# Performance work log

Hardware: AMD Instinct MI355X
Metric: run time of the kernel (lower is better)

Reference implementation:

```python
import jax, jax.numpy as jnp
import numpy as np

EPS = 1e-5

def _silu(x):
    return x * jax.nn.sigmoid(x)

def _layernorm(x, g, b):
    mu = jnp.mean(x, axis=-1, keepdims=True)
    var = jnp.mean((x - mu) ** 2, axis=-1, keepdims=True)
    return (x - mu) * jax.lax.rsqrt(var + EPS) * g + b

def _mamba(x, in_w, conv_w, conv_b, xproj_w, dt_w, dt_b, A_log, Dp, out_w):
    # x: (B, L, dm); faithful mamba-ssm block: in_proj -> causal dwconv -> silu ->
    # x_proj -> softplus(dt_proj) -> selective scan -> gate -> out_proj
    B, L, dm = x.shape
    di, K = conv_w.shape          # d_inner, d_conv
    ds = A_log.shape[1]           # d_state
    dtr = dt_w.shape[1]           # dt_rank
    xz = x @ in_w.T               # (B, L, 2*di)
    xi, z = jnp.split(xz, 2, axis=-1)
    # causal depthwise conv1d (pad K-1 on the left), kernel unrolled (K=4)
    xpad = jnp.pad(xi, ((0, 0), (K - 1, 0), (0, 0)))
    xc = conv_b + sum(conv_w[:, k] * xpad[:, k:k + L, :] for k in range(K))
    xc = _silu(xc)                # (B, L, di)
    xdbl = xc @ xproj_w.T         # (B, L, dtr + 2*ds)
    dt, Bm, Cm = jnp.split(xdbl, [dtr, dtr + ds], axis=-1)
    delta = jax.nn.softplus(dt @ dt_w.T + dt_b)        # (B, L, di)
    A = -jnp.exp(A_log)                                # (di, ds)
    dA = jnp.exp(delta[..., None] * A)                 # (B, L, di, ds)
    dBu = delta[..., None] * Bm[:, :, None, :] * xc[..., None]
    def step(h, inp):
        dA_t, dBu_t, C_t = inp                         # (B,di,ds),(B,di,ds),(B,ds)
        h = dA_t * h + dBu_t
        y = jnp.einsum('bdn,bn->bd', h, C_t)
        return h, y
    h0 = jnp.zeros((B, di, ds), dtype=x.dtype)
    _, ys = jax.lax.scan(step, h0, (dA.transpose(1, 0, 2, 3),
                                    dBu.transpose(1, 0, 2, 3),
                                    Cm.transpose(1, 0, 2)))
    y = ys.transpose(1, 0, 2) + xc * Dp                # (B, L, di)
    y = y * _silu(z)
    return y @ out_w.T                                 # (B, L, dm)

def _forward(t1, t2, t3, t4, t5,
             m0_in_w, m0_conv_w, m0_conv_b, m0_xproj_w, m0_dt_w, m0_dt_b, m0_Alog, m0_D, m0_out_w,
             m1_in_w, m1_conv_w, m1_conv_b, m1_xproj_w, m1_dt_w, m1_dt_b, m1_Alog, m1_D, m1_out_w,
             norm_g, norm_b, proj_w, proj_b, norm1_g, norm1_b, proj1_w, proj1_b, skip_scale):
    B = t1.shape[0]
    flat = lambda t, c: t.reshape(B, c, -1).transpose(0, 2, 1)   # (B, N, C)
    f1, f2, f3, f4, f5 = flat(t1, 8), flat(t2, 16), flat(t3, 24), flat(t4, 32), flat(t5, 48)
    c1 = jnp.concatenate([f1[:, :, 0:8], f2[:, :, 0:8], f3[:, :, 0:8], f4[:, :, 0:8], f5[:, :, 0:8]], axis=1)   # (B,21824,8)
    c2 = jnp.concatenate([f2[:, :, 8:16], f3[:, :, 8:16], f4[:, :, 8:16], f5[:, :, 8:16]], axis=1)              # (B,5440,8)
    c3 = jnp.concatenate([f3[:, :, 16:24], f4[:, :, 16:24], f5[:, :, 16:24]], axis=1)                           # (B,1344,8)
    c4 = jnp.concatenate([f4[:, :, 24:32], f5[:, :, 24:32]], axis=1)                                            # (B,320,8)
    c5 = f5[:, :, 32:48]                                                                                        # (B,64,16)
    def block8(c):
        y = _mamba(c, m0_in_w, m0_conv_w, m0_conv_b, m0_xproj_w, m0_dt_w, m0_dt_b, m0_Alog, m0_D, m0_out_w)
        return _layernorm(y + skip_scale * c, norm_g, norm_b) @ proj_w.T + proj_b
    x1m, x2m, x3m, x4m = block8(c1), block8(c2), block8(c3), block8(c4)
    y5 = _mamba(c5, m1_in_w, m1_conv_w, m1_conv_b, m1_xproj_w, m1_dt_w, m1_dt_b, m1_Alog, m1_D, m1_out_w)
    x5m = _layernorm(y5 + skip_scale * c5, norm1_g, norm1_b) @ proj1_w.T + proj1_b
    a1 = x1m[:, 0:16384, :]
    a2 = jnp.concatenate([x1m[:, 16384:20480, :], x2m[:, 0:4096, :]], axis=2)
    a3 = jnp.concatenate([x1m[:, 20480:21504, :], x2m[:, 4096:5120, :], x3m[:, 0:1024, :]], axis=2)
    a4 = jnp.concatenate([x1m[:, 21504:21760, :], x2m[:, 5120:5376, :], x3m[:, 1024:1280, :], x4m[:, 0:256, :]], axis=2)
    a5 = jnp.concatenate([x1m[:, 21760:, :], x2m[:, 5376:, :], x3m[:, 1280:, :], x4m[:, 256:, :], x5m], axis=2)
    x1 = a1.transpose(0, 2, 1).reshape(B, 8, 128, 128)
    x2 = a2.transpose(0, 2, 1).reshape(B, 16, 64, 64)
    x3 = a3.transpose(0, 2, 1).reshape(B, 24, 32, 32)
    x4 = a4.transpose(0, 2, 1).reshape(B, 32, 16, 16)
    x5 = a5.transpose(0, 2, 1).reshape(B, 48, 8, 8)
    return (x1, x2, x3, x4, x5)

def setup_inputs() -> dict:
    key = jax.random.key(0)
    ks = iter(jax.random.split(key, 64))
    B = 8
    def n(shape, s=1.0):
        return jax.random.normal(next(ks), shape, dtype=jnp.float32) * s
    inp = {
        't1': n((B, 8, 128, 128)), 't2': n((B, 16, 64, 64)), 't3': n((B, 24, 32, 32)),
        't4': n((B, 32, 16, 16)), 't5': n((B, 48, 8, 8)),
    }
    def mamba_params(pfx, dm):
        di, ds, K, dtr = 2 * dm, 16, 4, 1  # expand=2, d_state=16, d_conv=4, dt_rank=ceil(dm/16)=1
        return {
            pfx + '_in_w': n((2 * di, dm), dm ** -0.5),
            pfx + '_conv_w': n((di, K), 0.3),
            pfx + '_conv_b': n((di,), 0.1),
            pfx + '_xproj_w': n((dtr + 2 * ds, di), di ** -0.5),
            pfx + '_dt_w': n((di, dtr), 1.0),
            pfx + '_dt_b': n((di,), 0.1) - 3.0,
            pfx + '_Alog': jnp.log(jnp.tile(jnp.arange(1.0, ds + 1.0, dtype=jnp.float32), (di, 1))),
            pfx + '_D': jnp.ones((di,), jnp.float32),
            pfx + '_out_w': n((dm, di), di ** -0.5),
        }
    inp.update(mamba_params('m0', 8))
    inp.update(mamba_params('m1', 16))
    inp.update({
        'norm_g': jnp.ones((8,), jnp.float32), 'norm_b': jnp.zeros((8,), jnp.float32),
        'proj_w': n((8, 8), 8 ** -0.5), 'proj_b': jnp.zeros((8,), jnp.float32),
        'norm1_g': jnp.ones((16,), jnp.float32), 'norm1_b': jnp.zeros((16,), jnp.float32),
        'proj1_w': n((16, 16), 16 ** -0.5), 'proj1_b': jnp.zeros((16,), jnp.float32),
        'skip_scale': jnp.ones((1,), jnp.float32),
    })
    return inp

def reference(t1, t2, t3, t4, t5,
              m0_in_w, m0_conv_w, m0_conv_b, m0_xproj_w, m0_dt_w, m0_dt_b, m0_Alog, m0_D, m0_out_w,
              m1_in_w, m1_conv_w, m1_conv_b, m1_xproj_w, m1_dt_w, m1_dt_b, m1_Alog, m1_D, m1_out_w,
              norm_g, norm_b, proj_w, proj_b, norm1_g, norm1_b, proj1_w, proj1_b, skip_scale):
    return _forward(t1, t2, t3, t4, t5,
                    m0_in_w, m0_conv_w, m0_conv_b, m0_xproj_w, m0_dt_w, m0_dt_b, m0_Alog, m0_D, m0_out_w,
                    m1_in_w, m1_conv_w, m1_conv_b, m1_xproj_w, m1_dt_w, m1_dt_b, m1_Alog, m1_D, m1_out_w,
                    norm_g, norm_b, proj_w, proj_b, norm1_g, norm1_b, proj1_w, proj1_b, skip_scale)
```

## Files before the change

kernel.cpp:

```cpp
#include <hip/hip_runtime.h>
#include <cmath>

#define SCH 128
#define SUB 32
#define NCB 228
#define NCHUNK 1824
#define NSUB 7296
#define CPB3 2
#define NBLK3 912
#define LOG2E 1.442695041f
#define LN2F  0.6931471806f
#define EXP2F(x) __builtin_exp2f(x)
#define LOG2F(x) __builtin_log2f(x)
#define SW_IN 0
#define SW_CONVW 256
#define SW_CONVB 320
#define SW_XPROJ 336
#define SW_DTW 864
#define SW_DTB 880
#define SW_A 896
#define SW_D 1152
#define SW_OUTW 1168
#define SW_NG 1296
#define SW_NB 1304
#define SW_PW 1312
#define SW_PB 1376
#define SW_SKIP 1384
#define REC 1392
#define XP8 5872
#define GRECW 5004
#define YOF 6396
#define SMEMP1 6396
#define V_IN 0
#define V_CONVW 1024
#define V_CONVB 1152
#define V_XPROJ 1184
#define V_DTW 2240
#define V_DTB 2272
#define V_A 2304
#define V_D 2816
#define V_OUTW 2848
#define V_NG 3360
#define V_NB 3376
#define V_PW 3392
#define V_PB 3648
#define V_SKIP 3664
#define V_XC 3668
#define V_DL 5780
#define V_BM 7892
#define V_CM 8916
#define SMEM3 9940

struct Params {
  const float *t0, *t1, *t2, *t3, *t4;
  const float *in_w0,*conv_w0,*conv_b0,*xproj0,*dtw0,*dtb0,*Alog0,*D0,*outw0;
  const float *in_w1,*conv_w1,*conv_b1,*xproj1,*dtw1,*dtb1,*Alog1,*D1,*outw1;
  const float *ng,*nb,*pw,*pb,*n1g,*n1b,*p1w,*p1b,*skip;
  float* out;
  float *hloc, *sumdelta, *grec;
};

__device__ __forceinline__ float softplusf(float x) {
  float t = EXP2F(-fabsf(x) * LOG2E);
  return fmaxf(x, 0.f) + LOG2F(1.f + t) * LN2F;
}
__device__ __forceinline__ float siluf(float x) { return x * (1.f / (1.f + __expf(-x))); }
__device__ __forceinline__ unsigned pk(float a, float b) {
  unsigned ua = __float_as_uint(a) + 0x8000u;
  unsigned ub = __float_as_uint(b) + 0x8000u;
  return (ua >> 16) | (ub & 0xFFFF0000u);
}
__device__ __forceinline__ float lo16(unsigned w) { return __uint_as_float(w << 16); }
__device__ __forceinline__ float hi16(unsigned w) { return __uint_as_float(w & 0xFFFF0000u); }

struct Loc { int k, pos, ch, hw, C; };

__device__ __forceinline__ Loc locate(int seq, int l) {
  Loc r;
  if (seq == 0) { r.ch = 0;
    if (l < 16384)      { r.k=0; r.pos=l;        r.hw=16384; r.C=8;  }
    else if (l < 20480) { r.k=1; r.pos=l-16384;  r.hw=4096;  r.C=16; }
    else if (l < 21504) { r.k=2; r.pos=l-20480;  r.hw=1024;  r.C=24; }
    else if (l < 21760) { r.k=3; r.pos=l-21504;  r.hw=256;   r.C=32; }
    else                { r.k=4; r.pos=l-21760;  r.hw=64;    r.C=48; }
  } else if (seq == 1) { r.ch = 8;
    if (l < 4096)       { r.k=1; r.pos=l;        r.hw=4096;  r.C=16; }
    else if (l < 5120)  { r.k=2; r.pos=l-4096;   r.hw=1024;  r.C=24; }
    else if (l < 5376)  { r.k=3; r.pos=l-5120;   r.hw=256;   r.C=32; }
    else                { r.k=4; r.pos=l-5376;   r.hw=64;    r.C=48; }
  } else if (seq == 2) { r.ch = 16;
    if (l < 1024)       { r.k=2; r.pos=l;        r.hw=1024;  r.C=24; }
    else if (l < 1280)  { r.k=3; r.pos=l-1024;   r.hw=256;   r.C=32; }
    else                { r.k=4; r.pos=l-1280;   r.hw=64;    r.C=48; }
  } else { r.ch = 24;
    if (l < 256)        { r.k=3; r.pos=l;        r.hw=256;   r.C=32; }
    else                { r.k=4; r.pos=l-256;    r.hw=64;    r.C=48; }
  }
  return r;
}

__device__ __forceinline__ const float* tsel(const Params& p, int k) {
  switch (k) { case 0: return p.t0; case 1: return p.t1; case 2: return p.t2;
               case 3: return p.t3; default: return p.t4; }
}
__device__ __forceinline__ int outbase(int k) {
  switch (k) { case 0: return 0; case 1: return 1048576; case 2: return 1572864;
               case 3: return 1769472; default: return 1835008; }
}

__device__ __forceinline__ void gather8(const Params& p, int b, int seq, int l, float* c) {
  Loc lc = locate(seq, l);
  const float* t = tsel(p, lc.k);
  int base = (b * lc.C + lc.ch) * lc.hw + lc.pos;
  #pragma unroll
  for (int j = 0; j < 8; ++j) c[j] = t[base + j * lc.hw];
}

__device__ __forceinline__ void decode_bid(int bid, int& b, int& seq, int& l0, int& Sa) {
  b = bid / NCB;
  int r = bid - b * NCB;
  int c, L;
  if (r < 171)      { seq = 0; c = r;       L = 21824; }
  else if (r < 214) { seq = 1; c = r - 171; L = 5440;  }
  else if (r < 225) { seq = 2; c = r - 214; L = 1344;  }
  else              { seq = 3; c = r - 225; L = 320;   }
  l0 = c * SCH;
  int rem = L - l0;
  Sa = rem < SCH ? rem : SCH;
}

__device__ void load_w0(const Params& p, float* s, int tid) {
  for (int i = tid; i < 256; i += 256) s[SW_IN + i] = p.in_w0[i];
  for (int i = tid; i < 64;  i += 256) s[SW_CONVW + i] = p.conv_w0[i];
  for (int i = tid; i < 16;  i += 256) s[SW_CONVB + i] = p.conv_b0[i];
  for (int i = tid; i < 528; i += 256) s[SW_XPROJ + i] = p.xproj0[i];
  for (int i = tid; i < 16;  i += 256) s[SW_DTW + i] = p.dtw0[i];
  for (int i = tid; i < 16;  i += 256) s[SW_DTB + i] = p.dtb0[i];
  for (int i = tid; i < 256; i += 256) s[SW_A + i] = -__expf(p.Alog0[i]) * LOG2E;
  for (int i = tid; i < 16;  i += 256) s[SW_D + i] = p.D0[i];
  for (int i = tid; i < 128; i += 256) s[SW_OUTW + i] = p.outw0[i];
  for (int i = tid; i < 8;   i += 256) s[SW_NG + i] = p.ng[i];
  for (int i = tid; i < 8;   i += 256) s[SW_NB + i] = p.nb[i];
  for (int i = tid; i < 64;  i += 256) s[SW_PW + i] = p.pw[i];
  for (int i = tid; i < 8;   i += 256) s[SW_PB + i] = p.pb[i];
  if (tid == 0) s[SW_SKIP] = p.skip[0];
}

__device__ __forceinline__ float dot16h(const float* w, int ch0, int cho,
                                        const float* a, const float* o) {
  float4 wa0 = *(const float4*)&w[ch0];
  float4 wa1 = *(const float4*)&w[ch0 + 4];
  float4 wb0 = *(const float4*)&w[cho];
  float4 wb1 = *(const float4*)&w[cho + 4];
  float r = wa0.x * a[0];
  r = fmaf(wa0.y, a[1], r); r = fmaf(wa0.z, a[2], r); r = fmaf(wa0.w, a[3], r);
  r = fmaf(wa1.x, a[4], r); r = fmaf(wa1.y, a[5], r);
  r = fmaf(wa1.z, a[6], r); r = fmaf(wa1.w, a[7], r);
  r = fmaf(wb0.x, o[0], r); r = fmaf(wb0.y, o[1], r);
  r = fmaf(wb0.z, o[2], r); r = fmaf(wb0.w, o[3], r);
  r = fmaf(wb1.x, o[4], r); r = fmaf(wb1.y, o[5], r);
  r = fmaf(wb1.z, o[6], r); r = fmaf(wb1.w, o[7], r);
  return r;
}

__global__ __launch_bounds__(256, 6) void k_pass1(Params p) {
  __shared__ float s[SMEMP1];
  int tid = threadIdx.x;
  int cid = blockIdx.x;
  int b, seq, l0, Sa;
  decode_bid(cid, b, seq, l0, Sa);
  int tok = tid >> 1, hf = tid & 1;
  int ch0 = hf * 8, cho = 8 - ch0;
  bool act = tok < Sa;
  bool grow = tok < Sa + 3;
  bool hrow = (Sa == SCH) && (tok >= SCH - 3);
  float x8[8], x8h[8];
  {
    int l = l0 - 3 + tok;
    if (grow && l >= 0) gather8(p, b, seq, l, x8);
    else {
      #pragma unroll
      for (int j = 0; j < 8; ++j) x8[j] = 0.f;
    }
  }
  if (hrow) gather8(p, b, seq, l0 + tok, x8h);
  load_w0(p, s, tid);
  __syncthreads();
  if (grow) {
    #pragma unroll
    for (int ii = 0; ii < 8; ++ii) {
      int i = ch0 + ii;
      float4 wa = *(const float4*)&s[SW_IN + i * 8];
      float4 wb = *(const float4*)&s[SW_IN + i * 8 + 4];
      float a = wa.x * x8[0];
      a = fmaf(wa.y, x8[1], a); a = fmaf(wa.z, x8[2], a); a = fmaf(wa.w, x8[3], a);
      a = fmaf(wb.x, x8[4], a); a = fmaf(wb.y, x8[5], a);
      a = fmaf(wb.z, x8[6], a); a = fmaf(wb.w, x8[7], a);
      s[REC + tok * 17 + i] = a;
    }
    if (hf == 0) {
      unsigned* xp = (unsigned*)&s[XP8 + tok * 4];
      #pragma unroll
      for (int q = 0; q < 4; ++q) xp[q] = pk(x8[2*q], x8[2*q + 1]);
    }
  }
  if (hrow) {
    int r = tok + 3;
    #pragma unroll
    for (int ii = 0; ii < 8; ++ii) {
      int i = ch0 + ii;
      float4 wa = *(const float4*)&s[SW_IN + i * 8];
      float4 wb = *(const float4*)&s[SW_IN + i * 8 + 4];
      float a = wa.x * x8h[0];
      a = fmaf(wa.y, x8h[1], a); a = fmaf(wa.z, x8h[2], a); a = fmaf(wa.w, x8h[3], a);
      a = fmaf(wb.x, x8h[4], a); a = fmaf(wb.y, x8h[5], a);
      a = fmaf(wb.z, x8h[6], a); a = fmaf(wb.w, x8h[7], a);
      s[REC + r * 17 + i] = a;
    }
    if (hf == 0) {
      unsigned* xp = (unsigned*)&s[XP8 + r * 4];
      #pragma unroll
      for (int q = 0; q < 4; ++q) xp[q] = pk(x8h[2*q], x8h[2*q + 1]);
    }
  }
  __syncthreads();
  float xc8[8], xco[8];
  float dt = 0.f;
  if (act) {
    #pragma unroll
    for (int ii = 0; ii < 8; ++ii) {
      int i = ch0 + ii;
      float4 cw = *(const float4*)&s[SW_CONVW + i * 4];
      float a = s[SW_CONVB + i];
      a = fmaf(cw.x, s[REC + (tok + 0) * 17 + i], a);
      a = fmaf(cw.y, s[REC + (tok + 1) * 17 + i], a);
      a = fmaf(cw.z, s[REC + (tok + 2) * 17 + i], a);
      a = fmaf(cw.w, s[REC + (tok + 3) * 17 + i], a);
      xc8[ii] = siluf(a);
    }
    #pragma unroll
    for (int ii = 0; ii < 8; ++ii) xco[ii] = __shfl_xor(xc8[ii], 1);
    dt = dot16h(&s[SW_XPROJ], ch0, cho, xc8, xco);
  }
  __syncthreads();
  unsigned* ru = (unsigned*)&s[REC + tok * 35];
  if (act) {
    #pragma unroll
    for (int q = 0; q < 4; ++q) {
      int d0 = ch0 + 2 * q;
      float da = softplusf(fmaf(dt, s[SW_DTW + d0],     s[SW_DTB + d0]));
      float db = softplusf(fmaf(dt, s[SW_DTW + d0 + 1], s[SW_DTB + d0 + 1]));
      ru[hf * 4 + q]     = pk(da, db);
      ru[8 + hf * 4 + q] = pk(xc8[2*q], xc8[2*q + 1]);
    }
    #pragma unroll
    for (int q = 0; q < 4; ++q) {
      int n0 = ch0 + 2 * q;
      float a0 = dot16h(&s[SW_XPROJ + (1 + n0) * 16], ch0, cho, xc8, xco);
      float a1 = dot16h(&s[SW_XPROJ + (2 + n0) * 16], ch0, cho, xc8, xco);
      ru[16 + hf * 4 + q] = pk(a0, a1);
    }
    #pragma unroll
    for (int q = 0; q < 4; ++q) {
      int n0 = ch0 + 2 * q;
      float a0 = dot16h(&s[SW_XPROJ + (17 + n0) * 16], ch0, cho, xc8, xco);
      float a1 = dot16h(&s[SW_XPROJ + (18 + n0) * 16], ch0, cho, xc8, xco);
      ru[24 + hf * 4 + q] = pk(a0, a1);
    }
  } else {
    #pragma unroll
    for (int q = 0; q < 4; ++q) {
      ru[hf * 4 + q] = 0u;
      ru[8 + hf * 4 + q] = 0u;
      ru[16 + hf * 4 + q] = 0u;
      ru[24 + hf * 4 + q] = 0u;
    }
  }
  __syncthreads();
  const unsigned* su = (const unsigned*)s;
  {
    uint4* g4 = (uint4*)(p.grec + (size_t)cid * GRECW);
    const uint4* s4 = (const uint4*)&su[REC];
    #pragma unroll 2
    for (int i4 = tid; i4 < GRECW / 4; i4 += 256) g4[i4] = s4[i4];
  }
  int w = tid >> 6, lane = tid & 63;
  int d = lane >> 2, ng = lane & 3;
  int dh = d >> 1;
  bool dodd = d & 1;
  int t0 = w * SUB;
  float4 Av = *(float4*)&s[SW_A + d * 16 + ng * 4];
  float h0 = 0.f, h1 = 0.f, h2 = 0.f, h3 = 0.f, sd = 0.f;
  for (int tile = 0; tile < 8; ++tile) {
    int tb = t0 + tile * 4;
    unsigned wd[4], wx[4]; uint2 wB[4];
    #pragma unroll
    for (int i = 0; i < 4; ++i) {
      int base = REC + (tb + i) * 35;
      wd[i] = su[base + dh];
      wx[i] = su[base + 8 + dh];
      wB[i] = *(const uint2*)&su[base + 16 + ng * 2];
    }
    #pragma unroll
    for (int i = 0; i < 4; ++i) {
      float dl = dodd ? hi16(wd[i]) : lo16(wd[i]);
      float u = dl * (dodd ? hi16(wx[i]) : lo16(wx[i]));
      float e0 = EXP2F(Av.x * dl), e1 = EXP2F(Av.y * dl);
      float e2 = EXP2F(Av.z * dl), e3 = EXP2F(Av.w * dl);
      h0 = fmaf(e0, h0, u * lo16(wB[i].x));
      h1 = fmaf(e1, h1, u * hi16(wB[i].x));
      h2 = fmaf(e2, h2, u * lo16(wB[i].y));
      h3 = fmaf(e3, h3, u * hi16(wB[i].y));
      sd += dl;
    }
  }
  int gs = cid * 4 + w;
  unsigned* hu = (unsigned*)p.hloc;
  hu[gs * 128 + d * 8 + ng * 2]     = pk(h0, h1);
  hu[gs * 128 + d * 8 + ng * 2 + 1] = pk(h2, h3);
  if (ng == 0) p.sumdelta[(size_t)gs * 16 + d] = sd;
}

__device__ void load_w1(const Params& p, float* s, int tid) {
  for (int i = tid; i < 1024; i += 256) s[V_IN + i] = p.in_w1[i];
  for (int i = tid; i < 128;  i += 256) s[V_CONVW + i] = p.conv_w1[i];
  for (int i = tid; i < 32;   i += 256) s[V_CONVB + i] = p.conv_b1[i];
  for (int i = tid; i < 1056; i += 256) s[V_XPROJ + i] = p.xproj1[i];
  for (int i = tid; i < 32;   i += 256) s[V_DTW + i] = p.dtw1[i];
  for (int i = tid; i < 32;   i += 256) s[V_DTB + i] = p.dtb1[i];
  for (int i = tid; i < 512;  i += 256) s[V_A + i] = -__expf(p.Alog1[i]) * LOG2E;
  for (int i = tid; i < 32;   i += 256) s[V_D + i] = p.D1[i];
  for (int i = tid; i < 512;  i += 256) s[V_OUTW + i] = p.outw1[i];
  for (int i = tid; i < 16;   i += 256) s[V_NG + i] = p.n1g[i];
  for (int i = tid; i < 16;   i += 256) s[V_NB + i] = p.n1b[i];
  for (int i = tid; i < 256;  i += 256) s[V_PW + i] = p.p1w[i];
  for (int i = tid; i < 16;   i += 256) s[V_PB + i] = p.p1b[i];
  if (tid == 0) s[V_SKIP] = p.skip[0];
}

__device__ void c5_path(const Params& p, float* s, int b, int tid) {
  load_w1(p, s, tid);
  int og = tid >> 6, tok = tid & 63;
  float x16[16];
  #pragma unroll
  for (int j = 0; j < 16; ++j) x16[j] = p.t4[(b * 48 + 32 + j) * 64 + tok];
  __syncthreads();
  #pragma unroll
  for (int ii = 0; ii < 8; ++ii) {
    int i = og * 8 + ii;
    float a = 0.f;
    #pragma unroll
    for (int j = 0; j < 16; ++j) a = fmaf(s[V_IN + i * 16 + j], x16[j], a);
    float xm1 = __shfl_up(a, 1);
    float xm2 = __shfl_up(a, 2);
    float xm3 = __shfl_up(a, 3);
    float c = s[V_CONVB + i];
    c = fmaf(s[V_CONVW + i * 4 + 3], a, c);
    if (tok >= 1) c = fmaf(s[V_CONVW + i * 4 + 2], xm1, c);
    if (tok >= 2) c = fmaf(s[V_CONVW + i * 4 + 1], xm2, c);
    if (tok >= 3) c = fmaf(s[V_CONVW + i * 4 + 0], xm3, c);
    s[V_XC + tok * 33 + i] = siluf(c);
  }
  __syncthreads();
  float xcr[32];
  #pragma unroll
  for (int i = 0; i < 32; ++i) xcr[i] = s[V_XC + tok * 33 + i];
  float dt = 0.f;
  #pragma unroll
  for (int i = 0; i < 32; ++i) dt = fmaf(s[V_XPROJ + i], xcr[i], dt);
  #pragma unroll
  for (int nn = 0; nn < 4; ++nn) {
    int n = og * 4 + nn;
    float aB = 0.f, aC = 0.f;
    #pragma unroll
    for (int i = 0; i < 32; ++i) {
      aB = fmaf(s[V_XPROJ + (1 + n) * 32 + i], xcr[i], aB);
      aC = fmaf(s[V_XPROJ + (17 + n) * 32 + i], xcr[i], aC);
    }
    s[V_BM + tok * 16 + n] = aB;
    s[V_CM + tok * 16 + n] = aC;
  }
  #pragma unroll
  for (int ii = 0; ii < 8; ++ii) {
    int d = og * 8 + ii;
    s[V_DL + tok * 33 + d] = softplusf(fmaf(dt, s[V_DTW + d], s[V_DTB + d]));
  }
  __syncthreads();
  if (tid < 128) {
    int d = tid >> 2, ng = tid & 3;
    float4 Av = *(float4*)&s[V_A + d * 16 + ng * 4];
    float h0 = 0.f, h1 = 0.f, h2 = 0.f, h3 = 0.f;
    for (int tile = 0; tile < 16; ++tile) {
      int tb = tile * 4;
      float dl[4], xv[4]; float4 bm[4], cm[4];
      #pragma unroll
      for (int i = 0; i < 4; ++i) {
        dl[i] = s[V_DL + (tb + i) * 33 + d];
        xv[i] = s[V_XC + (tb + i) * 33 + d];
        bm[i] = *(float4*)&s[V_BM + (tb + i) * 16 + ng * 4];
        cm[i] = *(float4*)&s[V_CM + (tb + i) * 16 + ng * 4];
      }
      float yp[4];
      #pragma unroll
      for (int i = 0; i < 4; ++i) {
        float u = dl[i] * xv[i];
        float e0 = EXP2F(Av.x * dl[i]), e1 = EXP2F(Av.y * dl[i]);
        float e2 = EXP2F(Av.z * dl[i]), e3 = EXP2F(Av.w * dl[i]);
        h0 = fmaf(e0, h0, u * bm[i].x);
        h1 = fmaf(e1, h1, u * bm[i].y);
        h2 = fmaf(e2, h2, u * bm[i].z);
        h3 = fmaf(e3, h3, u * bm[i].w);
        float y = h0 * cm[i].x;
        y = fmaf(h1, cm[i].y, y); y = fmaf(h2, cm[i].z, y); y = fmaf(h3, cm[i].w, y);
        yp[i] = y;
      }
      #pragma unroll
      for (int i = 0; i < 4; ++i) yp[i] += __shfl_xor(yp[i], 1);
      #pragma unroll
      for (int i = 0; i < 4; ++i) yp[i] += __shfl_xor(yp[i], 2);
      float ysel = ng == 0 ? yp[0] : ng == 1 ? yp[1] : ng == 2 ? yp[2] : yp[3];
      s[V_DL + (tb + ng) * 33 + d] = ysel;
    }
  }
  __syncthreads();
  #pragma unroll
  for (int ii = 0; ii < 8; ++ii) {
    int d = og * 8 + ii;
    float z = 0.f;
    #pragma unroll
    for (int j = 0; j < 16; ++j) z = fmaf(s[V_IN + (32 + d) * 16 + j], x16[j], z);
    float yv = (s[V_DL + tok * 33 + d] + s[V_XC + tok * 33 + d] * s[V_D + d]) * siluf(z);
    s[V_DL + tok * 33 + d] = yv;
  }
  __syncthreads();
  float yr[32];
  #pragma unroll
  for (int d = 0; d < 32; ++d) yr[d] = s[V_DL + tok * 33 + d];
  float sk = s[V_SKIP];
  #pragma unroll
  for (int mm = 0; mm < 4; ++mm) {
    int m = og * 4 + mm;
    float a = sk * x16[m];
    #pragma unroll
    for (int d = 0; d < 32; ++d) a = fmaf(s[V_OUTW + m * 32 + d], yr[d], a);
    s[V_XC + tok * 33 + m] = a;
  }
  __syncthreads();
  if (tid < 64) {
    float ov[16];
    #pragma unroll
    for (int m = 0; m < 16; ++m) ov[m] = s[V_XC + tok * 33 + m];
    float mu = 0.f;
    #pragma unroll
    for (int m = 0; m < 16; ++m) mu += ov[m];
    mu *= (1.f / 16.f);
    float var = 0.f;
    #pragma unroll
    for (int m = 0; m < 16; ++m) { float t = ov[m] - mu; var += t * t; }
    var *= (1.f / 16.f);
    float inv = rsqrtf(var + 1e-5f);
    #pragma unroll
    for (int m = 0; m < 16; ++m)
      s[V_XC + tok * 33 + m] = (ov[m] - mu) * inv * s[V_NG + m] + s[V_NB + m];
  }
  __syncthreads();
  float lr[16];
  #pragma unroll
  for (int j = 0; j < 16; ++j) lr[j] = s[V_XC + tok * 33 + j];
  #pragma unroll
  for (int mm = 0; mm < 4; ++mm) {
    int m = og * 4 + mm;
    float a = s[V_PB + m];
    #pragma unroll
    for (int j = 0; j < 16; ++j) a = fmaf(s[V_PW + m * 16 + j], lr[j], a);
    p.out[1835008 + (b * 48 + 32 + m) * 64 + tok] = a;
  }
}

__global__ __launch_bounds__(256) void k_pass2(Params p) {
  __shared__ unsigned sh[684 * 8];
  __shared__ float ssd[684];
  __shared__ float sS[32];
  __shared__ float sH[512];
  int bid = blockIdx.x, tid = threadIdx.x;
  int b = bid >> 6;
  int rr = bid & 63;
  int seq = rr >> 4, d = rr & 15;
  const int nch[4] = {171, 43, 11, 3};
  const int chf[4] = {0, 171, 214, 225};
  int nsub = nch[seq] * 4;
  int g0 = (b * NCB + chf[seq]) * 4;
  unsigned* hu = (unsigned*)p.hloc;
  int n8 = nsub * 8;
  for (int wdx = tid; wdx < n8; wdx += 256) {
    int rec = wdx >> 3, pr_ = wdx & 7;
    sh[wdx] = hu[(size_t)(g0 + rec) * 128 + d * 8 + pr_];
  }
  for (int rec = tid; rec < nsub; rec += 256)
    ssd[rec] = p.sumdelta[(size_t)(g0 + rec) * 16 + d];
  int g = tid >> 3, pr = tid & 7;
  float A0 = -__expf(p.Alog0[d * 16 + pr * 2]) * LOG2E;
  float A1 = -__expf(p.Alog0[d * 16 + pr * 2 + 1]) * LOG2E;
  __syncthreads();
  int T = (nsub + 31) >> 5;
  int i0 = g * T;
  int i1 = i0 + T; if (i1 > nsub) i1 = nsub;
  float S = 0.f, h0 = 0.f, h1 = 0.f;
  for (int i = i0; i < i1; ++i) {
    unsigned wl = sh[i * 8 + pr];
    float sv = ssd[i];
    float e0 = EXP2F(A0 * sv), e1 = EXP2F(A1 * sv);
    h0 = fmaf(e0, h0, lo16(wl));
    h1 = fmaf(e1, h1, hi16(wl));
    S += sv;
  }
  if (pr == 0) sS[g] = S;
  sH[g * 16 + pr * 2]     = h0;
  sH[g * 16 + pr * 2 + 1] = h1;
  __syncthreads();
  float q0 = 0.f, q1 = 0.f;
  for (int j = 0; j < g; ++j) {
    float Sj = sS[j];
    float e0 = EXP2F(A0 * Sj), e1 = EXP2F(A1 * Sj);
    q0 = fmaf(e0, q0, sH[j * 16 + pr * 2]);
    q1 = fmaf(e1, q1, sH[j * 16 + pr * 2 + 1]);
  }
  for (int i = i0; i < i1; ++i) {
    unsigned wl = sh[i * 8 + pr];
    float sv = ssd[i];
    sh[i * 8 + pr] = pk(q0, q1);
    float e0 = EXP2F(A0 * sv), e1 = EXP2F(A1 * sv);
    q0 = fmaf(e0, q0, lo16(wl));
    q1 = fmaf(e1, q1, hi16(wl));
  }
  __syncthreads();
  for (int wdx = tid; wdx < n8; wdx += 256) {
    int rec = wdx >> 3, pr_ = wdx & 7;
    hu[(size_t)(g0 + rec) * 128 + d * 8 + pr_] = sh[wdx];
  }
}

__global__ __launch_bounds__(256, 4) void k_pass3(Params p) {
  __shared__ float s[SMEM3];
  int tid = threadIdx.x;
  if (blockIdx.x < 8) { c5_path(p, s, blockIdx.x, tid); return; }
  load_w0(p, s, tid);
  int w = tid >> 6, lane = tid & 63;
  int d = lane >> 2, ng = lane & 3;
  int dh = d >> 1;
  bool dodd = d & 1;
  int t0 = w * SUB;
  int tok = tid >> 1, hf = tid & 1, ch0 = hf * 8;
  const unsigned* su = (const unsigned*)s;
  for (int it = 0; it < CPB3; ++it) {
    int cid = (blockIdx.x - 8) * CPB3 + it;
    int b, seq, l0, Sa;
    decode_bid(cid, b, seq, l0, Sa);
    __syncthreads();
    {
      const uint4* g4 = (const uint4*)(p.grec + (size_t)cid * GRECW);
      uint4* s4 = (uint4*)&((unsigned*)s)[REC];
      #pragma unroll 2
      for (int i4 = tid; i4 < GRECW / 4; i4 += 256) s4[i4] = g4[i4];
    }
    __syncthreads();
    int gs = cid * 4 + w;
    float4 Av = *(float4*)&s[SW_A + d * 16 + ng * 4];
    const unsigned* hu = (const unsigned*)p.hloc;
    unsigned hw0 = hu[gs * 128 + d * 8 + ng * 2];
    unsigned hw1 = hu[gs * 128 + d * 8 + ng * 2 + 1];
    float h0 = lo16(hw0), h1 = hi16(hw0), h2 = lo16(hw1), h3 = hi16(hw1);
    for (int tile = 0; tile < 8; ++tile) {
      int tb = t0 + tile * 4;
      unsigned wd[4], wx[4]; uint2 wB[4], wC[4];
      #pragma unroll
      for (int i = 0; i < 4; ++i) {
        int base = REC + (tb + i) * 35;
        wd[i] = su[base + dh];
        wx[i] = su[base + 8 + dh];
        wB[i] = *(const uint2*)&su[base + 16 + ng * 2];
        wC[i] = *(const uint2*)&su[base + 24 + ng * 2];
      }
      float yp[4];
      #pragma unroll
      for (int i = 0; i < 4; ++i) {
        float dl = dodd ? hi16(wd[i]) : lo16(wd[i]);
        float u = dl * (dodd ? hi16(wx[i]) : lo16(wx[i]));
        float e0 = EXP2F(Av.x * dl), e1 = EXP2F(Av.y * dl);
        float e2 = EXP2F(Av.z * dl), e3 = EXP2F(Av.w * dl);
        h0 = fmaf(e0, h0, u * lo16(wB[i].x));
        h1 = fmaf(e1, h1, u * hi16(wB[i].x));
        h2 = fmaf(e2, h2, u * lo16(wB[i].y));
        h3 = fmaf(e3, h3, u * hi16(wB[i].y));
        float y = h0 * lo16(wC[i].x);
        y = fmaf(h1, hi16(wC[i].x), y);
        y = fmaf(h2, lo16(wC[i].y), y);
        y = fmaf(h3, hi16(wC[i].y), y);
        yp[i] = y;
      }
      #pragma unroll
      for (int i = 0; i < 4; ++i) yp[i] += __shfl_xor(yp[i], 1);
      #pragma unroll
      for (int i = 0; i < 4; ++i) yp[i] += __shfl_xor(yp[i], 2);
      float ysel = ng == 0 ? yp[0] : ng == 1 ? yp[1] : ng == 2 ? yp[2] : yp[3];
      s[YOF + (tb + ng) * 17 + d] = ysel;
    }
    __syncthreads();
    if (tok < Sa) {
      const unsigned* xp = (const unsigned*)&s[XP8 + (tok + 3) * 4];
      float c8[8];
      #pragma unroll
      for (int q = 0; q < 4; ++q) { c8[2*q] = lo16(xp[q]); c8[2*q+1] = hi16(xp[q]); }
      const unsigned* ru = (const unsigned*)&s[REC + tok * 35];
      float yv8[8];
      #pragma unroll
      for (int q = 0; q < 4; ++q) {
        unsigned wv = ru[8 + hf * 4 + q];
        int d0 = ch0 + 2 * q;
        float4 w0a = *(const float4*)&s[SW_IN + (16 + d0) * 8];
        float4 w0b = *(const float4*)&s[SW_IN + (16 + d0) * 8 + 4];
        float4 w1a = *(const float4*)&s[SW_IN + (17 + d0) * 8];
        float4 w1b = *(const float4*)&s[SW_IN + (17 + d0) * 8 + 4];
        float z0 = w0a.x * c8[0];
        z0 = fmaf(w0a.y, c8[1], z0); z0 = fmaf(w0a.z, c8[2], z0); z0 = fmaf(w0a.w, c8[3], z0);
        z0 = fmaf(w0b.x, c8[4], z0); z0 = fmaf(w0b.y, c8[5], z0);
        z0 = fmaf(w0b.z, c8[6], z0); z0 = fmaf(w0b.w, c8[7], z0);
        float z1 = w1a.x * c8[0];
        z1 = fmaf(w1a.y, c8[1], z1); z1 = fmaf(w1a.z, c8[2], z1); z1 = fmaf(w1a.w, c8[3], z1);
        z1 = fmaf(w1b.x, c8[4], z1); z1 = fmaf(w1b.y, c8[5], z1);
        z1 = fmaf(w1b.z, c8[6], z1); z1 = fmaf(w1b.w, c8[7], z1);
        yv8[2*q]   = (s[YOF + tok * 17 + d0]     + lo16(wv) * s[SW_D + d0])     * siluf(z0);
        yv8[2*q+1] = (s[YOF + tok * 17 + d0 + 1] + hi16(wv) * s[SW_D + d0 + 1]) * siluf(z1);
      }
      float o[8];
      float sk = s[SW_SKIP];
      #pragma unroll
      for (int m = 0; m < 8; ++m) {
        float4 wv0 = *(const float4*)&s[SW_OUTW + m * 16 + ch0];
        float4 wv1 = *(const float4*)&s[SW_OUTW + m * 16 + ch0 + 4];
        float a = wv0.x * yv8[0];
        a = fmaf(wv0.y, yv8[1], a); a = fmaf(wv0.z, yv8[2], a); a = fmaf(wv0.w, yv8[3], a);
        a = fmaf(wv1.x, yv8[4], a); a = fmaf(wv1.y, yv8[5], a);
        a = fmaf(wv1.z, yv8[6], a); a = fmaf(wv1.w, yv8[7], a);
        a += __shfl_xor(a, 1);
        o[m] = a + sk * c8[m];
      }
      float mu = 0.f;
      #pragma unroll
      for (int m = 0; m < 8; ++m) mu += o[m];
      mu *= 0.125f;
      float var = 0.f;
      #pragma unroll
      for (int m = 0; m < 8; ++m) { float t = o[m] - mu; var += t * t; }
      var *= 0.125f;
      float inv = rsqrtf(var + 1e-5f);
      #pragma unroll
      for (int m = 0; m < 8; ++m) o[m] = (o[m] - mu) * inv * s[SW_NG + m] + s[SW_NB + m];
      Loc lc = locate(seq, l0 + tok);
      int obase = outbase(lc.k) + (b * lc.C + lc.ch) * lc.hw + lc.pos;
      #pragma unroll
      for (int mm = 0; mm < 4; ++mm) {
        int m = hf * 4 + mm;
        float4 pw0 = *(const float4*)&s[SW_PW + m * 8];
        float4 pw1 = *(const float4*)&s[SW_PW + m * 8 + 4];
        float a = s[SW_PB + m];
        a = fmaf(pw0.x, o[0], a); a = fmaf(pw0.y, o[1], a);
        a = fmaf(pw0.z, o[2], a); a = fmaf(pw0.w, o[3], a);
        a = fmaf(pw1.x, o[4], a); a = fmaf(pw1.y, o[5], a);
        a = fmaf(pw1.z, o[6], a); a = fmaf(pw1.w, o[7], a);
        p.out[obase + m * lc.hw] = a;
      }
    }
  }
}

extern "C" void kernel_launch(void* const* d_in, const int* in_sizes, int n_in,
                              void* d_out, int out_size, void* d_ws, size_t ws_size,
                              hipStream_t stream) {
  (void)in_sizes; (void)n_in; (void)out_size; (void)ws_size;
  Params p;
  p.t0 = (const float*)d_in[0];  p.t1 = (const float*)d_in[1];
  p.t2 = (const float*)d_in[2];  p.t3 = (const float*)d_in[3];
  p.t4 = (const float*)d_in[4];
  p.in_w0   = (const float*)d_in[5];
  p.conv_w0 = (const float*)d_in[6];
  p.conv_b0 = (const float*)d_in[7];
  p.xproj0  = (const float*)d_in[8];
  p.dtw0    = (const float*)d_in[9];
  p.dtb0    = (const float*)d_in[10];
  p.Alog0   = (const float*)d_in[11];
  p.D0      = (const float*)d_in[12];
  p.outw0   = (const float*)d_in[13];
  p.in_w1   = (const float*)d_in[14];
  p.conv_w1 = (const float*)d_in[15];
  p.conv_b1 = (const float*)d_in[16];
  p.xproj1  = (const float*)d_in[17];
  p.dtw1    = (const float*)d_in[18];
  p.dtb1    = (const float*)d_in[19];
  p.Alog1   = (const float*)d_in[20];
  p.D1      = (const float*)d_in[21];
  p.outw1   = (const float*)d_in[22];
  p.ng  = (const float*)d_in[23];
  p.nb  = (const float*)d_in[24];
  p.pw  = (const float*)d_in[25];
  p.pb  = (const float*)d_in[26];
  p.n1g = (const float*)d_in[27];
  p.n1b = (const float*)d_in[28];
  p.p1w = (const float*)d_in[29];
  p.p1b = (const float*)d_in[30];
  p.skip = (const float*)d_in[31];
  p.out = (float*)d_out;
  float* ws = (float*)d_ws;
  p.hloc     = ws;
  p.sumdelta = ws + (size_t)NSUB * 128;
  p.grec     = ws + (size_t)NSUB * 128 + (size_t)NSUB * 16;
  k_pass1<<<dim3(NCHUNK), dim3(256), 0, stream>>>(p);
  k_pass2<<<dim3(512), dim3(256), 0, stream>>>(p);
  k_pass3<<<dim3(NBLK3 + 8), dim3(256), 0, stream>>>(p);
}
```

Baseline: 124.1 us.

## Shrink pass1 LDS by writing C and raw inputs directly to global record

Pass1 no longer stages the C projection and packed input rows in shared memory. It writes them straight to the global per-chunk record, which shrinks the shared row stride and the total LDS, and the launch bound rises to 8 blocks per CU. Pass3 now handles one chunk per block instead of two and launches NCHUNK blocks, loading C and the inputs from separate regions of the record. This aims to raise occupancy and parallelism, at the cost of more scattered global stores in pass1 and more block-launch overhead in pass3.

```diff
diff --git a/kernel.cpp b/kernel.cpp
--- a/kernel.cpp
+++ b/kernel.cpp
@@ -6,8 +6,6 @@
 #define NCB 228
 #define NCHUNK 1824
 #define NSUB 7296
-#define CPB3 2
-#define NBLK3 912
 #define LOG2E 1.442695041f
 #define LN2F  0.6931471806f
 #define EXP2F(x) __builtin_exp2f(x)
@@ -27,10 +25,14 @@
 #define SW_PB 1376
 #define SW_SKIP 1384
 #define REC 1392
-#define XP8 5872
-#define GRECW 5004
-#define YOF 6396
-#define SMEMP1 6396
+#define RSTR 25
+#define GR_C 3200
+#define GR_X8 4224
+#define GRECW 4736
+#define SMEMP1 4592
+#define C3 4592
+#define X83 5616
+#define YOF 6128
 #define V_IN 0
 #define V_CONVW 1024
 #define V_CONVB 1152
@@ -163,7 +165,7 @@
   return r;
 }
 
-__global__ __launch_bounds__(256, 6) void k_pass1(Params p) {
+__global__ __launch_bounds__(256, 8) void k_pass1(Params p) {
   __shared__ float s[SMEMP1];
   int tid = threadIdx.x;
   int cid = blockIdx.x;
@@ -174,6 +176,7 @@
   bool act = tok < Sa;
   bool grow = tok < Sa + 3;
   bool hrow = (Sa == SCH) && (tok >= SCH - 3);
+  unsigned* gc = (unsigned*)(p.grec + (size_t)cid * GRECW);
   float x8[8], x8h[8];
   {
     int l = l0 - 3 + tok;
@@ -185,6 +188,18 @@
   }
   if (hrow) gather8(p, b, seq, l0 + tok, x8h);
   load_w0(p, s, tid);
+  if (hf == 0) {
+    if (grow && tok >= 3) {
+      uint4 v = make_uint4(pk(x8[0], x8[1]), pk(x8[2], x8[3]),
+                           pk(x8[4], x8[5]), pk(x8[6], x8[7]));
+      *(uint4*)&gc[GR_X8 + (tok - 3) * 4] = v;
+    }
+    if (hrow) {
+      uint4 v = make_uint4(pk(x8h[0], x8h[1]), pk(x8h[2], x8h[3]),
+                           pk(x8h[4], x8h[5]), pk(x8h[6], x8h[7]));
+      *(uint4*)&gc[GR_X8 + tok * 4] = v;
+    }
+  }
   __syncthreads();
   if (grow) {
     #pragma unroll
@@ -198,11 +213,6 @@
       a = fmaf(wb.z, x8[6], a); a = fmaf(wb.w, x8[7], a);
       s[REC + tok * 17 + i] = a;
     }
-    if (hf == 0) {
-      unsigned* xp = (unsigned*)&s[XP8 + tok * 4];
-      #pragma unroll
-      for (int q = 0; q < 4; ++q) xp[q] = pk(x8[2*q], x8[2*q + 1]);
-    }
   }
   if (hrow) {
     int r = tok + 3;
@@ -217,11 +227,6 @@
       a = fmaf(wb.z, x8h[6], a); a = fmaf(wb.w, x8h[7], a);
       s[REC + r * 17 + i] = a;
     }
-    if (hf == 0) {
-      unsigned* xp = (unsigned*)&s[XP8 + r * 4];
-      #pragma unroll
-      for (int q = 0; q < 4; ++q) xp[q] = pk(x8h[2*q], x8h[2*q + 1]);
-    }
   }
   __syncthreads();
   float xc8[8], xco[8];
@@ -243,7 +248,7 @@
     dt = dot16h(&s[SW_XPROJ], ch0, cho, xc8, xco);
   }
   __syncthreads();
-  unsigned* ru = (unsigned*)&s[REC + tok * 35];
+  unsigned* ru = (unsigned*)&s[REC + tok * RSTR];
   if (act) {
     #pragma unroll
     for (int q = 0; q < 4; ++q) {
@@ -260,29 +265,36 @@
       float a1 = dot16h(&s[SW_XPROJ + (2 + n0) * 16], ch0, cho, xc8, xco);
       ru[16 + hf * 4 + q] = pk(a0, a1);
     }
-    #pragma unroll
-    for (int q = 0; q < 4; ++q) {
-      int n0 = ch0 + 2 * q;
+    uint4 cv;
+    {
+      int n0 = ch0;
       float a0 = dot16h(&s[SW_XPROJ + (17 + n0) * 16], ch0, cho, xc8, xco);
       float a1 = dot16h(&s[SW_XPROJ + (18 + n0) * 16], ch0, cho, xc8, xco);
-      ru[24 + hf * 4 + q] = pk(a0, a1);
-    }
+      float a2 = dot16h(&s[SW_XPROJ + (19 + n0) * 16], ch0, cho, xc8, xco);
+      float a3 = dot16h(&s[SW_XPROJ + (20 + n0) * 16], ch0, cho, xc8, xco);
+      float a4 = dot16h(&s[SW_XPROJ + (21 + n0) * 16], ch0, cho, xc8, xco);
+      float a5 = dot16h(&s[SW_XPROJ + (22 + n0) * 16], ch0, cho, xc8, xco);
+      float a6 = dot16h(&s[SW_XPROJ + (23 + n0) * 16], ch0, cho, xc8, xco);
+      float a7 = dot16h(&s[SW_XPROJ + (24 + n0) * 16], ch0, cho, xc8, xco);
+      cv = make_uint4(pk(a0, a1), pk(a2, a3), pk(a4, a5), pk(a6, a7));
+    }
+    *(uint4*)&gc[GR_C + tok * 8 + hf * 4] = cv;
   } else {
     #pragma unroll
     for (int q = 0; q < 4; ++q) {
       ru[hf * 4 + q] = 0u;
       ru[8 + hf * 4 + q] = 0u;
       ru[16 + hf * 4 + q] = 0u;
-      ru[24 + hf * 4 + q] = 0u;
-    }
+    }
+    *(uint4*)&gc[GR_C + tok * 8 + hf * 4] = make_uint4(0u, 0u, 0u, 0u);
   }
   __syncthreads();
   const unsigned* su = (const unsigned*)s;
   {
-    uint4* g4 = (uint4*)(p.grec + (size_t)cid * GRECW);
+    uint4* g4 = (uint4*)gc;
     const uint4* s4 = (const uint4*)&su[REC];
     #pragma unroll 2
-    for (int i4 = tid; i4 < GRECW / 4; i4 += 256) g4[i4] = s4[i4];
+    for (int i4 = tid; i4 < GR_C / 4; i4 += 256) g4[i4] = s4[i4];
   }
   int w = tid >> 6, lane = tid & 63;
   int d = lane >> 2, ng = lane & 3;
@@ -296,7 +308,7 @@
     unsigned wd[4], wx[4]; uint2 wB[4];
     #pragma unroll
     for (int i = 0; i < 4; ++i) {
-      int base = REC + (tb + i) * 35;
+      int base = REC + (tb + i) * RSTR;
       wd[i] = su[base + dh];
       wx[i] = su[base + 8 + dh];
       wB[i] = *(const uint2*)&su[base + 16 + ng * 2];
@@ -552,124 +564,121 @@
   int t0 = w * SUB;
   int tok = tid >> 1, hf = tid & 1, ch0 = hf * 8;
   const unsigned* su = (const unsigned*)s;
-  for (int it = 0; it < CPB3; ++it) {
-    int cid = (blockIdx.x - 8) * CPB3 + it;
-    int b, seq, l0, Sa;
-    decode_bid(cid, b, seq, l0, Sa);
-    __syncthreads();
-    {
-      const uint4* g4 = (const uint4*)(p.grec + (size_t)cid * GRECW);
-      uint4* s4 = (uint4*)&((unsigned*)s)[REC];
-      #pragma unroll 2
-      for (int i4 = tid; i4 < GRECW / 4; i4 += 256) s4[i4] = g4[i4];
-    }
-    __syncthreads();
-    int gs = cid * 4 + w;
-    float4 Av = *(float4*)&s[SW_A + d * 16 + ng * 4];
-    const unsigned* hu = (const unsigned*)p.hloc;
-    unsigned hw0 = hu[gs * 128 + d * 8 + ng * 2];
-    unsigned hw1 = hu[gs * 128 + d * 8 + ng * 2 + 1];
-    float h0 = lo16(hw0), h1 = hi16(hw0), h2 = lo16(hw1), h3 = hi16(hw1);
-    for (int tile = 0; tile < 8; ++tile) {
-      int tb = t0 + tile * 4;
-      unsigned wd[4], wx[4]; uint2 wB[4], wC[4];
-      #pragma unroll
-      for (int i = 0; i < 4; ++i) {
-        int base = REC + (tb + i) * 35;
-        wd[i] = su[base + dh];
-        wx[i] = su[base + 8 + dh];
-        wB[i] = *(const uint2*)&su[base + 16 + ng * 2];
-        wC[i] = *(const uint2*)&su[base + 24 + ng * 2];
-      }
-      float yp[4];
-      #pragma unroll
-      for (int i = 0; i < 4; ++i) {
-        float dl = dodd ? hi16(wd[i]) : lo16(wd[i]);
-        float u = dl * (dodd ? hi16(wx[i]) : lo16(wx[i]));
-        float e0 = EXP2F(Av.x * dl), e1 = EXP2F(Av.y * dl);
-        float e2 = EXP2F(Av.z * dl), e3 = EXP2F(Av.w * dl);
-        h0 = fmaf(e0, h0, u * lo16(wB[i].x));
-        h1 = fmaf(e1, h1, u * hi16(wB[i].x));
-        h2 = fmaf(e2, h2, u * lo16(wB[i].y));
-        h3 = fmaf(e3, h3, u * hi16(wB[i].y));
-        float y = h0 * lo16(wC[i].x);
-        y = fmaf(h1, hi16(wC[i].x), y);
-        y = fmaf(h2, lo16(wC[i].y), y);
-        y = fmaf(h3, hi16(wC[i].y), y);
-        yp[i] = y;
-      }
-      #pragma unroll
-      for (int i = 0; i < 4; ++i) yp[i] += __shfl_xor(yp[i], 1);
-      #pragma unroll
-      for (int i = 0; i < 4; ++i) yp[i] += __shfl_xor(yp[i], 2);
-      float ysel = ng == 0 ? yp[0] : ng == 1 ? yp[1] : ng == 2 ? yp[2] : yp[3];
-      s[YOF + (tb + ng) * 17 + d] = ysel;
-    }
-    __syncthreads();
-    if (tok < Sa) {
-      const unsigned* xp = (const unsigned*)&s[XP8 + (tok + 3) * 4];
-      float c8[8];
-      #pragma unroll
-      for (int q = 0; q < 4; ++q) { c8[2*q] = lo16(xp[q]); c8[2*q+1] = hi16(xp[q]); }
-      const unsigned* ru = (const unsigned*)&s[REC + tok * 35];
-      float yv8[8];
-      #pragma unroll
-      for (int q = 0; q < 4; ++q) {
-        unsigned wv = ru[8 + hf * 4 + q];
-        int d0 = ch0 + 2 * q;
-        float4 w0a = *(const float4*)&s[SW_IN + (16 + d0) * 8];
-        float4 w0b = *(const float4*)&s[SW_IN + (16 + d0) * 8 + 4];
-        float4 w1a = *(const float4*)&s[SW_IN + (17 + d0) * 8];
-        float4 w1b = *(const float4*)&s[SW_IN + (17 + d0) * 8 + 4];
-        float z0 = w0a.x * c8[0];
-        z0 = fmaf(w0a.y, c8[1], z0); z0 = fmaf(w0a.z, c8[2], z0); z0 = fmaf(w0a.w, c8[3], z0);
-        z0 = fmaf(w0b.x, c8[4], z0); z0 = fmaf(w0b.y, c8[5], z0);
-        z0 = fmaf(w0b.z, c8[6], z0); z0 = fmaf(w0b.w, c8[7], z0);
-        float z1 = w1a.x * c8[0];
-        z1 = fmaf(w1a.y, c8[1], z1); z1 = fmaf(w1a.z, c8[2], z1); z1 = fmaf(w1a.w, c8[3], z1);
-        z1 = fmaf(w1b.x, c8[4], z1); z1 = fmaf(w1b.y, c8[5], z1);
-        z1 = fmaf(w1b.z, c8[6], z1); z1 = fmaf(w1b.w, c8[7], z1);
-        yv8[2*q]   = (s[YOF + tok * 17 + d0]     + lo16(wv) * s[SW_D + d0])     * siluf(z0);
-        yv8[2*q+1] = (s[YOF + tok * 17 + d0 + 1] + hi16(wv) * s[SW_D + d0 + 1]) * siluf(z1);
-      }
-      float o[8];
-      float sk = s[SW_SKIP];
-      #pragma unroll
-      for (int m = 0; m < 8; ++m) {
-        float4 wv0 = *(const float4*)&s[SW_OUTW + m * 16 + ch0];
-        float4 wv1 = *(const float4*)&s[SW_OUTW + m * 16 + ch0 + 4];
-        float a = wv0.x * yv8[0];
-        a = fmaf(wv0.y, yv8[1], a); a = fmaf(wv0.z, yv8[2], a); a = fmaf(wv0.w, yv8[3], a);
-        a = fmaf(wv1.x, yv8[4], a); a = fmaf(wv1.y, yv8[5], a);
-        a = fmaf(wv1.z, yv8[6], a); a = fmaf(wv1.w, yv8[7], a);
-        a += __shfl_xor(a, 1);
-        o[m] = a + sk * c8[m];
-      }
-      float mu = 0.f;
-      #pragma unroll
-      for (int m = 0; m < 8; ++m) mu += o[m];
-      mu *= 0.125f;
-      float var = 0.f;
-      #pragma unroll
-      for (int m = 0; m < 8; ++m) { float t = o[m] - mu; var += t * t; }
-      var *= 0.125f;
-      float inv = rsqrtf(var + 1e-5f);
-      #pragma unroll
-      for (int m = 0; m < 8; ++m) o[m] = (o[m] - mu) * inv * s[SW_NG + m] + s[SW_NB + m];
-      Loc lc = locate(seq, l0 + tok);
-      int obase = outbase(lc.k) + (b * lc.C + lc.ch) * lc.hw + lc.pos;
-      #pragma unroll
-      for (int mm = 0; mm < 4; ++mm) {
-        int m = hf * 4 + mm;
-        float4 pw0 = *(const float4*)&s[SW_PW + m * 8];
-        float4 pw1 = *(const float4*)&s[SW_PW + m * 8 + 4];
-        float a = s[SW_PB + m];
-        a = fmaf(pw0.x, o[0], a); a = fmaf(pw0.y, o[1], a);
-        a = fmaf(pw0.z, o[2], a); a = fmaf(pw0.w, o[3], a);
-        a = fmaf(pw1.x, o[4], a); a = fmaf(pw1.y, o[5], a);
-        a = fmaf(pw1.z, o[6], a); a = fmaf(pw1.w, o[7], a);
-        p.out[obase + m * lc.hw] = a;
-      }
+  int cid = blockIdx.x - 8;
+  int b, seq, l0, Sa;
+  decode_bid(cid, b, seq, l0, Sa);
+  {
+    const uint4* g4 = (const uint4*)(p.grec + (size_t)cid * GRECW);
+    uint4* s4 = (uint4*)&((unsigned*)s)[REC];
+    #pragma unroll 2
+    for (int i4 = tid; i4 < GRECW / 4; i4 += 256) s4[i4] = g4[i4];
+  }
+  __syncthreads();
+  int gs = cid * 4 + w;
+  float4 Av = *(float4*)&s[SW_A + d * 16 + ng * 4];
+  const unsigned* hu = (const unsigned*)p.hloc;
+  unsigned hw0 = hu[gs * 128 + d * 8 + ng * 2];
+  unsigned hw1 = hu[gs * 128 + d * 8 + ng * 2 + 1];
+  float h0 = lo16(hw0), h1 = hi16(hw0), h2 = lo16(hw1), h3 = hi16(hw1);
+  for (int tile = 0; tile < 8; ++tile) {
+    int tb = t0 + tile * 4;
+    unsigned wd[4], wx[4]; uint2 wB[4], wC[4];
+    #pragma unroll
+    for (int i = 0; i < 4; ++i) {
+      int base = REC + (tb + i) * RSTR;
+      wd[i] = su[base + dh];
+      wx[i] = su[base + 8 + dh];
+      wB[i] = *(const uint2*)&su[base + 16 + ng * 2];
+      wC[i] = *(const uint2*)&su[C3 + (tb + i) * 8 + ng * 2];
+    }
+    float yp[4];
+    #pragma unroll
+    for (int i = 0; i < 4; ++i) {
+      float dl = dodd ? hi16(wd[i]) : lo16(wd[i]);
+      float u = dl * (dodd ? hi16(wx[i]) : lo16(wx[i]));
+      float e0 = EXP2F(Av.x * dl), e1 = EXP2F(Av.y * dl);
+      float e2 = EXP2F(Av.z * dl), e3 = EXP2F(Av.w * dl);
+      h0 = fmaf(e0, h0, u * lo16(wB[i].x));
+      h1 = fmaf(e1, h1, u * hi16(wB[i].x));
+      h2 = fmaf(e2, h2, u * lo16(wB[i].y));
+      h3 = fmaf(e3, h3, u * hi16(wB[i].y));
+      float y = h0 * lo16(wC[i].x);
+      y = fmaf(h1, hi16(wC[i].x), y);
+      y = fmaf(h2, lo16(wC[i].y), y);
+      y = fmaf(h3, hi16(wC[i].y), y);
+      yp[i] = y;
+    }
+    #pragma unroll
+    for (int i = 0; i < 4; ++i) yp[i] += __shfl_xor(yp[i], 1);
+    #pragma unroll
+    for (int i = 0; i < 4; ++i) yp[i] += __shfl_xor(yp[i], 2);
+    float ysel = ng == 0 ? yp[0] : ng == 1 ? yp[1] : ng == 2 ? yp[2] : yp[3];
+    s[YOF + (tb + ng) * 17 + d] = ysel;
+  }
+  __syncthreads();
+  if (tok < Sa) {
+    const unsigned* xp = (const unsigned*)&s[X83 + tok * 4];
+    float c8[8];
+    #pragma unroll
+    for (int q = 0; q < 4; ++q) { c8[2*q] = lo16(xp[q]); c8[2*q+1] = hi16(xp[q]); }
+    const unsigned* ru = (const unsigned*)&s[REC + tok * RSTR];
+    float yv8[8];
+    #pragma unroll
+    for (int q = 0; q < 4; ++q) {
+      unsigned wv = ru[8 + hf * 4 + q];
+      int d0 = ch0 + 2 * q;
+      float4 w0a = *(const float4*)&s[SW_IN + (16 + d0) * 8];
+      float4 w0b = *(const float4*)&s[SW_IN + (16 + d0) * 8 + 4];
+      float4 w1a = *(const float4*)&s[SW_IN + (17 + d0) * 8];
+      float4 w1b = *(const float4*)&s[SW_IN + (17 + d0) * 8 + 4];
+      float z0 = w0a.x * c8[0];
+      z0 = fmaf(w0a.y, c8[1], z0); z0 = fmaf(w0a.z, c8[2], z0); z0 = fmaf(w0a.w, c8[3], z0);
+      z0 = fmaf(w0b.x, c8[4], z0); z0 = fmaf(w0b.y, c8[5], z0);
+      z0 = fmaf(w0b.z, c8[6], z0); z0 = fmaf(w0b.w, c8[7], z0);
+      float z1 = w1a.x * c8[0];
+      z1 = fmaf(w1a.y, c8[1], z1); z1 = fmaf(w1a.z, c8[2], z1); z1 = fmaf(w1a.w, c8[3], z1);
+      z1 = fmaf(w1b.x, c8[4], z1); z1 = fmaf(w1b.y, c8[5], z1);
+      z1 = fmaf(w1b.z, c8[6], z1); z1 = fmaf(w1b.w, c8[7], z1);
+      yv8[2*q]   = (s[YOF + tok * 17 + d0]     + lo16(wv) * s[SW_D + d0])     * siluf(z0);
+      yv8[2*q+1] = (s[YOF + tok * 17 + d0 + 1] + hi16(wv) * s[SW_D + d0 + 1]) * siluf(z1);
+    }
+    float o[8];
+    float sk = s[SW_SKIP];
+    #pragma unroll
+    for (int m = 0; m < 8; ++m) {
+      float4 wv0 = *(const float4*)&s[SW_OUTW + m * 16 + ch0];
+      float4 wv1 = *(const float4*)&s[SW_OUTW + m * 16 + ch0 + 4];
+      float a = wv0.x * yv8[0];
+      a = fmaf(wv0.y, yv8[1], a); a = fmaf(wv0.z, yv8[2], a); a = fmaf(wv0.w, yv8[3], a);
+      a = fmaf(wv1.x, yv8[4], a); a = fmaf(wv1.y, yv8[5], a);
+      a = fmaf(wv1.z, yv8[6], a); a = fmaf(wv1.w, yv8[7], a);
+      a += __shfl_xor(a, 1);
+      o[m] = a + sk * c8[m];
+    }
+    float mu = 0.f;
+    #pragma unroll
+    for (int m = 0; m < 8; ++m) mu += o[m];
+    mu *= 0.125f;
+    float var = 0.f;
+    #pragma unroll
+    for (int m = 0; m < 8; ++m) { float t = o[m] - mu; var += t * t; }
+    var *= 0.125f;
+    float inv = rsqrtf(var + 1e-5f);
+    #pragma unroll
+    for (int m = 0; m < 8; ++m) o[m] = (o[m] - mu) * inv * s[SW_NG + m] + s[SW_NB + m];
+    Loc lc = locate(seq, l0 + tok);
+    int obase = outbase(lc.k) + (b * lc.C + lc.ch) * lc.hw + lc.pos;
+    #pragma unroll
+    for (int mm = 0; mm < 4; ++mm) {
+      int m = hf * 4 + mm;
+      float4 pw0 = *(const float4*)&s[SW_PW + m * 8];
+      float4 pw1 = *(const float4*)&s[SW_PW + m * 8 + 4];
+      float a = s[SW_PB + m];
+      a = fmaf(pw0.x, o[0], a); a = fmaf(pw0.y, o[1], a);
+      a = fmaf(pw0.z, o[2], a); a = fmaf(pw0.w, o[3], a);
+      a = fmaf(pw1.x, o[4], a); a = fmaf(pw1.y, o[5], a);
+      a = fmaf(pw1.z, o[6], a); a = fmaf(pw1.w, o[7], a);
+      p.out[obase + m * lc.hw] = a;
     }
   }
 }
@@ -716,5 +725,5 @@
   p.grec     = ws + (size_t)NSUB * 128 + (size_t)NSUB * 16;
   k_pass1<<<dim3(NCHUNK), dim3(256), 0, stream>>>(p);
   k_pass2<<<dim3(512), dim3(256), 0, stream>>>(p);
-  k_pass3<<<dim3(NBLK3 + 8), dim3(256), 0, stream>>>(p);
-}
+  k_pass3<<<dim3(NCHUNK + 8), dim3(256), 0, stream>>>(p);
+}
```

Result: faster. 113.9 us (-8.2%).
